# Optimization experiments

Measured on AMD Instinct MI355X. Metric: run time of the kernel, lower is better.

Reference implementation:

```python
import jax, jax.numpy as jnp
import numpy as np

IN_DIM = 256
OUT_DIM = 256
EMBED_DIM = 256
GROUPS = 8
BN_EPS = 1e-5


def conv2d(x, w, b, pad, groups=1):
    # x: NCHW, w: OIHW (I = in_ch / groups)
    out = jax.lax.conv_general_dilated(
        x, w, window_strides=(1, 1), padding=[(pad, pad), (pad, pad)],
        dimension_numbers=('NCHW', 'OIHW', 'NCHW'), feature_group_count=groups)
    return out + b[None, :, None, None]


def setup_inputs() -> dict:
    key = jax.random.key(0)
    ks = jax.random.split(key, 8)
    s = 0.05
    d = {}
    d['x'] = jax.random.normal(ks[0], (2, IN_DIM, 16, 16), jnp.float32)
    d['y'] = jax.random.normal(ks[1], (2, OUT_DIM, 128, 128), jnp.float32)
    # channle_reduce: Conv2d(256, 64, k=3, groups=64) -> weight (64, 4, 3, 3)
    d['w_cr'] = jax.random.normal(ks[2], (IN_DIM // 4, 4, 3, 3), jnp.float32) * s
    d['b_cr'] = jnp.zeros((IN_DIM // 4,), jnp.float32)
    # depthwise convs on 64 channels
    d['w_dw3'] = jax.random.normal(ks[3], (IN_DIM // 4, 1, 3, 3), jnp.float32) * s
    d['b_dw3'] = jnp.zeros((IN_DIM // 4,), jnp.float32)
    d['w_dw7'] = jax.random.normal(ks[4], (IN_DIM // 4, 1, 5, 5), jnp.float32) * s
    d['b_dw7'] = jnp.zeros((IN_DIM // 4,), jnp.float32)
    # gate: Conv2d(256, 128, 1) + BN + StarReLU
    d['w_gate'] = jax.random.normal(ks[5], (IN_DIM // 2, IN_DIM, 1, 1), jnp.float32) * s
    d['b_gate'] = jnp.zeros((IN_DIM // 2,), jnp.float32)
    d['bn_gamma'] = jnp.ones((IN_DIM // 2,), jnp.float32)
    d['bn_beta'] = jnp.zeros((IN_DIM // 2,), jnp.float32)
    d['bn_mean'] = jnp.zeros((IN_DIM // 2,), jnp.float32)
    d['bn_var'] = jnp.ones((IN_DIM // 2,), jnp.float32)
    d['sr_scale'] = jnp.ones((1,), jnp.float32)
    d['sr_bias'] = jnp.zeros((1,), jnp.float32)
    # linear1: Linear(16, 8192) -> torch weight shape (8192, 16)
    d['w_lin'] = jax.random.normal(ks[6], (OUT_DIM * EMBED_DIM // GROUPS, IN_DIM // (2 * GROUPS)), jnp.float32) * s
    d['b_lin'] = jnp.zeros((OUT_DIM * EMBED_DIM // GROUPS,), jnp.float32)
    return d


def reference(x, y, w_cr, b_cr, w_dw3, b_dw3, w_dw7, b_dw7, w_gate, b_gate,
              bn_gamma, bn_beta, bn_mean, bn_var, sr_scale, sr_bias, w_lin, b_lin):
    B, C, H, Wd = x.shape
    # gate branch: 1x1 conv -> BN (inference stats) -> StarReLU
    g = conv2d(x, w_gate, b_gate, 0)
    inv = (bn_gamma / jnp.sqrt(bn_var + BN_EPS))[None, :, None, None]
    g = (g - bn_mean[None, :, None, None]) * inv + bn_beta[None, :, None, None]
    g = sr_scale * jnp.square(jnp.maximum(g, 0.0)) + sr_bias
    # feature branch
    xr = conv2d(x, w_cr, b_cr, 1, groups=IN_DIM // 4)        # (B, 64, H, W)
    x3 = conv2d(xr, w_dw3, b_dw3, 1, groups=IN_DIM // 4)
    x7 = conv2d(xr, w_dw7, b_dw7, 2, groups=IN_DIM // 4)
    xc = jnp.concatenate([x3, x7], axis=1) * g               # (B, 128, H, W)
    # per-pixel weight generation: (B,H,W,G,16) @ (16,8192)
    xc = xc.reshape(B, GROUPS, -1, H, Wd).transpose(0, 3, 4, 1, 2)
    wdec = jnp.einsum('bhwgi,oi->bhwgo', xc, w_lin) + b_lin  # (B,H,W,8,8192)
    # flatten (G, out*embed/G) -> (embed, out); matches torch reshape order
    wdec = wdec.reshape(B, H, Wd, EMBED_DIM, OUT_DIM)
    # patch-wise dynamic 1x1 conv == per-patch batched matmul
    b, c, h, w = y.shape
    fh, fw = H, Wd
    ph, pw = h // fh, w // fw
    yp = y.reshape(b, c, fh, ph, fw, pw)
    # out[b,e,f,p,g,q] = sum_c wdec[b,f,g,e,c] * y[b,c,f,p,g,q]
    out = jnp.einsum('bfgec,bcfpgq->befpgq', wdec, yp)
    return out.reshape(b, EMBED_DIM, h, w)
```

## Files before the change

### kernel.cpp

```cpp
#include <hip/hip_runtime.h>
#include <stdint.h>


typedef __attribute__((ext_vector_type(8))) short short8;
typedef __attribute__((ext_vector_type(4))) float f32x4;

#define BN_EPS 1e-5f

__device__ __forceinline__ unsigned short f2bf(float f) {
  unsigned u = __float_as_uint(f);
  return (unsigned short)((u + 0x8000u) >> 16);
}
__device__ __forceinline__ unsigned pk2bf(float a, float b) {
  unsigned ua = __float_as_uint(a), ub = __float_as_uint(b);
  return ((ua + 0x8000u) >> 16) | ((ub + 0x8000u) & 0xFFFF0000u);
}

__global__ __launch_bounds__(256) void k1a_groupconv(
    const float* __restrict__ x, const float* __restrict__ w_cr,
    const float* __restrict__ b_cr, float* __restrict__ xr)
{
  __shared__ float xs[4][256];
  int b = blockIdx.x >> 6, cr = blockIdx.x & 63;
  int t = threadIdx.x;
  {
    int ch = t >> 6, off = (t & 63) * 4;
    float4 v = *(const float4*)(x + b * 65536 + (cr * 4 + ch) * 256 + off);
    *(float4*)&xs[ch][off] = v;
  }
  __syncthreads();
  int h = t >> 4, w = t & 15;
  float a = b_cr[cr];
  #pragma unroll
  for (int ii = 0; ii < 4; ++ii) {
    const float* wp = w_cr + (cr * 4 + ii) * 9;
    #pragma unroll
    for (int ky = 0; ky < 3; ++ky) {
      int gy = h + ky - 1;
      #pragma unroll
      for (int kx = 0; kx < 3; ++kx) {
        int gx = w + kx - 1;
        float v = (gy >= 0 && gy < 16 && gx >= 0 && gx < 16) ? xs[ii][gy * 16 + gx] : 0.f;
        a += wp[ky * 3 + kx] * v;
      }
    }
  }
  xr[(b * 64 + cr) * 256 + t] = a;
}

__global__ __launch_bounds__(256) void k1b_gate_dw(
    const float* __restrict__ x, const float* __restrict__ xr,
    const float* __restrict__ w_dw3, const float* __restrict__ b_dw3,
    const float* __restrict__ w_dw7, const float* __restrict__ b_dw7,
    const float* __restrict__ w_gate, const float* __restrict__ b_gate,
    const float* __restrict__ bn_gamma, const float* __restrict__ bn_beta,
    const float* __restrict__ bn_mean, const float* __restrict__ bn_var,
    const float* __restrict__ sr_scale, const float* __restrict__ sr_bias,
    const float* __restrict__ w_lin, short* __restrict__ wlin_bf, short* __restrict__ xc_bf)
{
  __shared__ float xcen[256];
  __shared__ float gs[128];
  int blk = blockIdx.x;
  int b = blk >> 8, h = (blk >> 4) & 15, w = blk & 15;
  int t = threadIdx.x;

  { int idx = blk * 256 + t; wlin_bf[idx] = (short)f2bf(w_lin[idx]); }

  xcen[t] = x[b * 65536 + t * 256 + h * 16 + w];
  __syncthreads();

  int o = t >> 1, half = t & 1;
  {
    const float* wrow = w_gate + o * 256 + half * 128;
    const float* xcn  = xcen + half * 128;
    float ga = 0.f;
    #pragma unroll 8
    for (int ci = 0; ci < 128; ci += 4) {
      float4 wv = *(const float4*)(wrow + ci);
      float4 xv = *(const float4*)(xcn + ci);
      ga += wv.x * xv.x + wv.y * xv.y + wv.z * xv.z + wv.w * xv.w;
    }
    ga += __shfl_xor(ga, 1);
    float inv = bn_gamma[o] * rsqrtf(bn_var[o] + BN_EPS);
    float gg = (ga + b_gate[o] - bn_mean[o]) * inv + bn_beta[o];
    gg = fmaxf(gg, 0.f);
    gg = sr_scale[0] * gg * gg + sr_bias[0];
    if (half == 0) gs[o] = gg;
  }
  __syncthreads();

  if (t < 128) {
    int oc = t;
    float f0;
    if (oc < 64) {
      f0 = b_dw3[oc];
      const float* wp = w_dw3 + oc * 9;
      const float* xp = xr + (b * 64 + oc) * 256;
      #pragma unroll
      for (int ky = 0; ky < 3; ++ky) {
        int gy = h + ky - 1;
        #pragma unroll
        for (int kx = 0; kx < 3; ++kx) {
          int gx = w + kx - 1;
          float v = (gy >= 0 && gy < 16 && gx >= 0 && gx < 16) ? xp[gy * 16 + gx] : 0.f;
          f0 += wp[ky * 3 + kx] * v;
        }
      }
    } else {
      int c5 = oc - 64;
      f0 = b_dw7[c5];
      const float* wp = w_dw7 + c5 * 25;
      const float* xp = xr + (b * 64 + c5) * 256;
      #pragma unroll
      for (int ky = 0; ky < 5; ++ky) {
        int gy = h + ky - 2;
        #pragma unroll
        for (int kx = 0; kx < 5; ++kx) {
          int gx = w + kx - 2;
          float v = (gy >= 0 && gy < 16 && gx >= 0 && gx < 16) ? xp[gy * 5 * 0 + gy * 16 + gx] : 0.f;
          f0 += wp[ky * 5 + kx] * v;
        }
      }
    }
    int pix = (b * 16 + h) * 16 + w;
    xc_bf[pix * 128 + oc] = (short)f2bf(f0 * gs[oc]);
  }
}

__global__ __launch_bounds__(256) void k2a_wgen(
    const short* __restrict__ wlin_bf, const short* __restrict__ xc_bf,
    const float* __restrict__ b_lin, short* __restrict__ wd)
{
  int blk = blockIdx.x;
  int n0 = (blk >> 2) * 16;
  int tid = threadIdx.x;
  int wave = tid >> 6, lane = tid & 63;
  int quad = lane >> 4, l16 = lane & 15;
  int obase = (blk & 3) * 2048 + wave * 512;

  short8 af = {0, 0, 0, 0, 0, 0, 0, 0};
  if (quad < 2) af = *(const short8*)(xc_bf + (n0 + l16) * 16 + quad * 8);

  f32x4 zero4 = {0.f, 0.f, 0.f, 0.f};
  #pragma unroll 8
  for (int i = 0; i < 32; ++i) {
    int o0 = obase + i * 16;
    short8 bf = {0, 0, 0, 0, 0, 0, 0, 0};
    if (quad < 2) bf = *(const short8*)(wlin_bf + (o0 + l16) * 16 + quad * 8);
    f32x4 d = __builtin_amdgcn_mfma_f32_16x16x32_bf16(af, bf, zero4, 0, 0, 0);
    float bl = b_lin[o0 + l16];
    short* wp = wd + (size_t)(n0 + quad * 4) * 8192 + o0 + l16;
    #pragma unroll
    for (int r = 0; r < 4; ++r)
      wp[(size_t)r * 8192] = (short)f2bf(d[r] + bl);
  }
}

__global__ __launch_bounds__(512, 4) void k2b_dynconv(
    const float* __restrict__ y, const short* __restrict__ wd,
    float* __restrict__ out)
{
  __shared__ __align__(16) short Ylds[16384];
  __shared__ __align__(16) float scratch[8192];

  int phys = blockIdx.x;
  int blk = (phys & 7) * 64 + (phys >> 3);
  int b = blk >> 8, f = (blk >> 4) & 15, g = blk & 15;
  int tid = threadIdx.x;
  int wave = tid >> 6, lane = tid & 63;
  int quad = lane >> 4, l16 = lane & 15;

  const float* yb = y + b * 4194304 + (f * 8) * 128 + g * 8;
  const short* wdp = wd + (size_t)(((b * 16 + f) * 16 + g)) * 65536;

  int c32 = tid >> 4, pf = tid & 15;
  for (int sch = 0; sch < 2; ++sch) {
    float4 v[4];
    #pragma unroll
    for (int it = 0; it < 4; ++it)
      v[it] = *(const float4*)(yb + (sch * 128 + it * 32 + c32) * 16384 + (pf >> 1) * 128 + (pf & 1) * 4);
    #pragma unroll
    for (int it = 0; it < 4; ++it)
      *(float4*)&scratch[(it * 32 + c32) * 64 + pf * 4] = v[it];
    __syncthreads();
    #pragma unroll
    for (int tt = 0; tt < 2; ++tt) {
      int task = tt * 512 + tid;
      int pix = task & 63, cg = task >> 6;
      float s0 = scratch[(cg * 8 + 0) * 64 + pix];
      float s1 = scratch[(cg * 8 + 1) * 64 + pix];
      float s2 = scratch[(cg * 8 + 2) * 64 + pix];
      float s3 = scratch[(cg * 8 + 3) * 64 + pix];
      float s4 = scratch[(cg * 8 + 4) * 64 + pix];
      float s5 = scratch[(cg * 8 + 5) * 64 + pix];
      float s6 = scratch[(cg * 8 + 6) * 64 + pix];
      float s7 = scratch[(cg * 8 + 7) * 64 + pix];
      uint4 pk;
      pk.x = pk2bf(s0, s1); pk.y = pk2bf(s2, s3);
      pk.z = pk2bf(s4, s5); pk.w = pk2bf(s6, s7);
      int chunk = sch * 16 + cg;
      int physc = chunk ^ (pix & 7);
      *(uint4*)&Ylds[pix * 256 + physc * 8] = pk;
    }
    __syncthreads();
  }

  f32x4 acc[2][4];
  f32x4 zero4 = {0.f, 0.f, 0.f, 0.f};
  #pragma unroll
  for (int et = 0; et < 2; ++et)
    #pragma unroll
    for (int nt = 0; nt < 4; ++nt)
      acc[et][nt] = zero4;

  #pragma unroll 2
  for (int cc = 0; cc < 8; ++cc) {
    short8 A[2], Bf[4];
    #pragma unroll
    for (int et = 0; et < 2; ++et) {
      int e = wave * 32 + et * 16 + l16;
      A[et] = *(const short8*)(wdp + e * 256 + cc * 32 + quad * 8);
    }
    int chunk = cc * 4 + quad;
    #pragma unroll
    for (int nt = 0; nt < 4; ++nt) {
      int nn = nt * 16 + l16;
      int physc = chunk ^ (nn & 7);
      Bf[nt] = *(const short8*)&Ylds[nn * 256 + physc * 8];
    }
    #pragma unroll
    for (int et = 0; et < 2; ++et)
      #pragma unroll
      for (int nt = 0; nt < 4; ++nt)
        acc[et][nt] = __builtin_amdgcn_mfma_f32_16x16x32_bf16(A[et], Bf[nt], acc[et][nt], 0, 0, 0);
  }

  float* ob = out + b * 4194304 + (f * 8) * 128 + g * 8;
  #pragma unroll
  for (int et = 0; et < 2; ++et) {
    int e0 = wave * 32 + et * 16 + quad * 4;
    #pragma unroll
    for (int nt = 0; nt < 4; ++nt) {
      int pix = nt * 16 + l16;
      float* oa = ob + (pix >> 3) * 128 + (pix & 7);
      #pragma unroll
      for (int r = 0; r < 4; ++r)
        oa[(e0 + r) * 16384] = acc[et][nt][r];
    }
  }
}

extern "C" void kernel_launch(void* const* d_in, const int* in_sizes, int n_in,
                              void* d_out, int out_size, void* d_ws, size_t ws_size,
                              hipStream_t stream) {
  const float* x        = (const float*)d_in[0];
  const float* y        = (const float*)d_in[1];
  const float* w_cr     = (const float*)d_in[2];
  const float* b_cr     = (const float*)d_in[3];
  const float* w_dw3    = (const float*)d_in[4];
  const float* b_dw3    = (const float*)d_in[5];
  const float* w_dw7    = (const float*)d_in[6];
  const float* b_dw7    = (const float*)d_in[7];
  const float* w_gate   = (const float*)d_in[8];
  const float* b_gate   = (const float*)d_in[9];
  const float* bn_gamma = (const float*)d_in[10];
  const float* bn_beta  = (const float*)d_in[11];
  const float* bn_mean  = (const float*)d_in[12];
  const float* bn_var   = (const float*)d_in[13];
  const float* sr_scale = (const float*)d_in[14];
  const float* sr_bias  = (const float*)d_in[15];
  const float* w_lin    = (const float*)d_in[16];
  const float* b_lin    = (const float*)d_in[17];
  float* out = (float*)d_out;

  short* xc_bf   = (short*)d_ws;
  short* wlin_bf = (short*)((char*)d_ws + 131072);
  float* xr      = (float*)((char*)d_ws + 131072 + 262144);
  short* wd      = (short*)((char*)d_ws + 131072 + 262144 + 131072);

  hipLaunchKernelGGL(k1a_groupconv, dim3(128), dim3(256), 0, stream, x, w_cr, b_cr, xr);
  hipLaunchKernelGGL(k1b_gate_dw, dim3(512), dim3(256), 0, stream,
                     x, xr, w_dw3, b_dw3, w_dw7, b_dw7, w_gate, b_gate,
                     bn_gamma, bn_beta, bn_mean, bn_var, sr_scale, sr_bias,
                     w_lin, wlin_bf, xc_bf);
  hipLaunchKernelGGL(k2a_wgen, dim3(1024), dim3(256), 0, stream,
                     wlin_bf, xc_bf, b_lin, wd);
  hipLaunchKernelGGL(k2b_dynconv, dim3(512), dim3(512), 0, stream, y, wd, out);
}
```

Baseline: 162.4 us.

## Stage wgen output through LDS for coalesced stores; shrink dynconv scratch for occupancy

The weight-generation kernel now writes its MFMA results into a shared-memory tile and then stores it to global memory as contiguous 8-byte chunks, replacing scattered 2-byte stores. The dynamic-conv kernel halves its fp32 transpose scratch buffer, processes the y tile in four 64-channel passes with the next pass's global loads issued early, and raises the launch-bounds occupancy hint from 4 to 6 blocks. The aim is to cut uncoalesced write traffic and raise occupancy, at the cost of more barriers per block and extra shared memory in the wgen kernel.

```diff
diff --git a/kernel.cpp b/kernel.cpp
--- a/kernel.cpp
+++ b/kernel.cpp
@@ -117,7 +117,7 @@
         #pragma unroll
         for (int kx = 0; kx < 5; ++kx) {
           int gx = w + kx - 2;
-          float v = (gy >= 0 && gy < 16 && gx >= 0 && gx < 16) ? xp[gy * 5 * 0 + gy * 16 + gx] : 0.f;
+          float v = (gy >= 0 && gy < 16 && gx >= 0 && gx < 16) ? xp[gy * 16 + gx] : 0.f;
           f0 += wp[ky * 5 + kx] * v;
         }
       }
@@ -131,12 +131,13 @@
     const short* __restrict__ wlin_bf, const short* __restrict__ xc_bf,
     const float* __restrict__ b_lin, short* __restrict__ wd)
 {
+  __shared__ __align__(16) short Wt[16 * 2048];
   int blk = blockIdx.x;
   int n0 = (blk >> 2) * 16;
+  int oc = (blk & 3) * 2048;
   int tid = threadIdx.x;
   int wave = tid >> 6, lane = tid & 63;
   int quad = lane >> 4, l16 = lane & 15;
-  int obase = (blk & 3) * 2048 + wave * 512;
 
   short8 af = {0, 0, 0, 0, 0, 0, 0, 0};
   if (quad < 2) af = *(const short8*)(xc_bf + (n0 + l16) * 16 + quad * 8);
@@ -144,24 +145,33 @@
   f32x4 zero4 = {0.f, 0.f, 0.f, 0.f};
   #pragma unroll 8
   for (int i = 0; i < 32; ++i) {
-    int o0 = obase + i * 16;
+    int o0 = wave * 512 + i * 16;
     short8 bf = {0, 0, 0, 0, 0, 0, 0, 0};
-    if (quad < 2) bf = *(const short8*)(wlin_bf + (o0 + l16) * 16 + quad * 8);
+    if (quad < 2) bf = *(const short8*)(wlin_bf + (oc + o0 + l16) * 16 + quad * 8);
     f32x4 d = __builtin_amdgcn_mfma_f32_16x16x32_bf16(af, bf, zero4, 0, 0, 0);
-    float bl = b_lin[o0 + l16];
-    short* wp = wd + (size_t)(n0 + quad * 4) * 8192 + o0 + l16;
+    float bl = b_lin[oc + o0 + l16];
     #pragma unroll
     for (int r = 0; r < 4; ++r)
-      wp[(size_t)r * 8192] = (short)f2bf(d[r] + bl);
-  }
-}
-
-__global__ __launch_bounds__(512, 4) void k2b_dynconv(
+      Wt[(quad * 4 + r) * 2048 + o0 + l16] = (short)f2bf(d[r] + bl);
+  }
+  __syncthreads();
+
+  const uint2* src = (const uint2*)Wt;
+  #pragma unroll 8
+  for (int j = 0; j < 32; ++j) {
+    int fl = j * 256 + tid;
+    int row = fl >> 9;
+    int col = (fl & 511) * 4;
+    *(uint2*)(wd + (size_t)(n0 + row) * 8192 + oc + col) = src[fl];
+  }
+}
+
+__global__ __launch_bounds__(512, 6) void k2b_dynconv(
     const float* __restrict__ y, const short* __restrict__ wd,
     float* __restrict__ out)
 {
   __shared__ __align__(16) short Ylds[16384];
-  __shared__ __align__(16) float scratch[8192];
+  __shared__ __align__(16) float scratch[4096];
 
   int phys = blockIdx.x;
   int blk = (phys & 7) * 64 + (phys >> 3);
@@ -173,20 +183,31 @@
   const float* yb = y + b * 4194304 + (f * 8) * 128 + g * 8;
   const short* wdp = wd + (size_t)(((b * 16 + f) * 16 + g)) * 65536;
 
-  int c32 = tid >> 4, pf = tid & 15;
-  for (int sch = 0; sch < 2; ++sch) {
-    float4 v[4];
-    #pragma unroll
-    for (int it = 0; it < 4; ++it)
-      v[it] = *(const float4*)(yb + (sch * 128 + it * 32 + c32) * 16384 + (pf >> 1) * 128 + (pf & 1) * 4);
-    #pragma unroll
-    for (int it = 0; it < 4; ++it)
-      *(float4*)&scratch[(it * 32 + c32) * 64 + pf * 4] = v[it];
+  int c_a = (tid >> 4) & 63;
+  (void)c_a;
+  float4 v0, v1, w0, w1;
+  {
+    int task0 = tid, task1 = 512 + tid;
+    int ca = task0 >> 4, pfa = task0 & 15;
+    int cb = task1 >> 4, pfb = task1 & 15;
+    v0 = *(const float4*)(yb + ca * 16384 + (pfa >> 1) * 128 + (pfa & 1) * 4);
+    v1 = *(const float4*)(yb + cb * 16384 + (pfb >> 1) * 128 + (pfb & 1) * 4);
+  }
+  for (int pass = 0; pass < 4; ++pass) {
+    {
+      int task0 = tid, task1 = 512 + tid;
+      int ca = task0 >> 4, pfa = task0 & 15;
+      int cb = task1 >> 4, pfb = task1 & 15;
+      *(float4*)&scratch[ca * 64 + pfa * 4] = v0;
+      *(float4*)&scratch[cb * 64 + pfb * 4] = v1;
+      if (pass < 3) {
+        w0 = *(const float4*)(yb + ((pass + 1) * 64 + ca) * 16384 + (pfa >> 1) * 128 + (pfa & 1) * 4);
+        w1 = *(const float4*)(yb + ((pass + 1) * 64 + cb) * 16384 + (pfb >> 1) * 128 + (pfb & 1) * 4);
+      }
+    }
     __syncthreads();
-    #pragma unroll
-    for (int tt = 0; tt < 2; ++tt) {
-      int task = tt * 512 + tid;
-      int pix = task & 63, cg = task >> 6;
+    {
+      int pix = tid & 63, cg = tid >> 6;
       float s0 = scratch[(cg * 8 + 0) * 64 + pix];
       float s1 = scratch[(cg * 8 + 1) * 64 + pix];
       float s2 = scratch[(cg * 8 + 2) * 64 + pix];
@@ -198,11 +219,12 @@
       uint4 pk;
       pk.x = pk2bf(s0, s1); pk.y = pk2bf(s2, s3);
       pk.z = pk2bf(s4, s5); pk.w = pk2bf(s6, s7);
-      int chunk = sch * 16 + cg;
+      int chunk = pass * 8 + cg;
       int physc = chunk ^ (pix & 7);
       *(uint4*)&Ylds[pix * 256 + physc * 8] = pk;
     }
     __syncthreads();
+    v0 = w0; v1 = w1;
   }
 
   f32x4 acc[2][4];
```

Measured after the change: 174.5 us. 1.07x slower.
